# Optimization experiments

Hardware: AMD Instinct MI355X
Metric: run time of the kernel (lower is better)

The kernel has to match this reference:

```python
import jax, jax.numpy as jnp
import numpy as np

E, K, D, H, C = 32768, 32, 128, 4, 10
DH = D // H

def setup_inputs() -> dict:
    key = jax.random.key(0)
    ks = jax.random.split(key, 9)
    s = 1.0 / np.sqrt(D)
    return {
        "edge_feats": jax.random.normal(ks[0], (E, D), jnp.float32),
        "Wq": jax.random.normal(ks[1], (D, D), jnp.float32) * s,
        "Wk": jax.random.normal(ks[2], (D, D), jnp.float32) * s,
        "Wv": jax.random.normal(ks[3], (D, D), jnp.float32) * s,
        "Wo": jax.random.normal(ks[4], (D, D), jnp.float32) * s,
        "W1": jax.random.normal(ks[5], (D, D), jnp.float32) * s,
        "b1": jnp.zeros((D,), jnp.float32),
        "W2": jax.random.normal(ks[6], (D, C), jnp.float32) * s,
        "b2": jnp.zeros((C,), jnp.float32),
        "edge_adj": jax.random.randint(ks[7], (E, K), 0, E, jnp.int32),
    }

def reference(edge_feats, Wq, Wk, Wv, Wo, W1, b1, W2, b2, edge_adj):
    # Edge attention: each edge attends over its K adjacent edges.
    q = (edge_feats @ Wq).reshape(E, H, DH)                 # [E,H,dh]
    k_all = edge_feats @ Wk                                  # [E,D]
    v_all = edge_feats @ Wv                                  # [E,D]
    kn = k_all[edge_adj].reshape(E, K, H, DH)                # gather [E,K,H,dh]
    vn = v_all[edge_adj].reshape(E, K, H, DH)                # gather [E,K,H,dh]
    scores = jnp.einsum("ehd,ekhd->ehk", q, kn) / np.sqrt(DH)
    attn = jax.nn.softmax(scores, axis=-1)                   # [E,H,K]
    ctx = jnp.einsum("ehk,ekhd->ehd", attn, vn).reshape(E, D)
    edge_out = ctx @ Wo                                       # [E,D]
    # classifier: Linear -> GELU -> Linear
    h = jax.nn.gelu(edge_out @ W1 + b1)
    logits = h @ W2 + b2                                      # [E,C]
    return logits
```

## Files before the change

### kernel.cpp

```cpp
#include <hip/hip_runtime.h>
#include <hip/hip_bf16.h>

constexpr int E_EDGES = 32768;
constexpr int DIM = 128;

using bf16x8 = __attribute__((ext_vector_type(8))) short;
using f32x4  = __attribute__((ext_vector_type(4))) float;
using f32x2  = __attribute__((ext_vector_type(2))) float;
typedef unsigned int uint4v __attribute__((ext_vector_type(4)));
typedef unsigned int uint2v __attribute__((ext_vector_type(2)));

__device__ inline float bflo(unsigned u) { return __uint_as_float(u << 16); }
__device__ inline float bfhi(unsigned u) { return __uint_as_float(u & 0xffff0000u); }
__device__ inline f32x2 bf2f2(unsigned u) {
    f32x2 r;
    r[0] = __uint_as_float(u << 16);
    r[1] = __uint_as_float(u & 0xffff0000u);
    return r;
}
__device__ inline f32x2 fma2(f32x2 a, f32x2 b, f32x2 c) {
    return __builtin_elementwise_fma(a, b, c);
}
__device__ inline unsigned pk_bf2(float a, float b) {
    __hip_bfloat162 h = __float22bfloat162_rn(make_float2(a, b));
    return *(unsigned*)&h;
}

#if __has_builtin(__builtin_amdgcn_fdot2_f32_bf16)
typedef __bf16 bf16x2v __attribute__((ext_vector_type(2)));
__device__ inline float dot2bf(unsigned a, unsigned b, float c) {
    return __builtin_amdgcn_fdot2_f32_bf16(__builtin_bit_cast(bf16x2v, a),
                                           __builtin_bit_cast(bf16x2v, b),
                                           c, false);
}
#else
__device__ inline float dot2bf(unsigned a, unsigned b, float c) {
    float r = fmaf(bflo(a), bflo(b), c);
    return fmaf(bfhi(a), bfhi(b), r);
}
#endif

__global__ __launch_bounds__(256) void k_prep(
    const float* __restrict__ Wq, const float* __restrict__ Wk,
    const float* __restrict__ Wv, const float* __restrict__ Wo,
    const float* __restrict__ W1, __hip_bfloat16* __restrict__ Wt,
    __hip_bfloat16* __restrict__ wft) {
    const int b = blockIdx.x;
    const int t = threadIdx.x;
    if (b < 3) {
        const float* W = (b == 0) ? Wq : (b == 1) ? Wk : Wv;
        __hip_bfloat16* dst = Wt + b * 16384;
#pragma unroll
        for (int i = 0; i < 8; ++i) {
            int idx = i * 2048 + t * 8;
            int k = idx >> 7, n0 = idx & 127;
            float4 f0 = *(const float4*)(W + k * 128 + n0);
            float4 f1 = *(const float4*)(W + k * 128 + n0 + 4);
            float f[8] = {f0.x, f0.y, f0.z, f0.w, f1.x, f1.y, f1.z, f1.w};
#pragma unroll
            for (int j = 0; j < 8; ++j)
                dst[(n0 + j) * 128 + k] = __float2bfloat16(f[j]);
        }
    } else {
        int idx = (b - 3) * 256 + t;
        int r = idx >> 7, c = idx & 127;
        float acc = 0.f;
#pragma unroll 16
        for (int k = 0; k < 128; ++k)
            acc = fmaf(Wo[r * 128 + k], W1[k * 128 + c], acc);
        wft[c * 128 + r] = __float2bfloat16(acc);
    }
}

__global__ __launch_bounds__(256) void k_qkv(
    const float* __restrict__ feats, const __hip_bfloat16* __restrict__ Wt,
    __hip_bfloat16* __restrict__ qp, __hip_bfloat16* __restrict__ kp,
    __hip_bfloat16* __restrict__ vp) {
    __shared__ short Als[16384];
    __shared__ short Bls[16384];

    const int t = threadIdx.x;
    const int lane = t & 63;
    const int w = t >> 6;
    const int wm = w >> 1, wn = w & 1;
    const int row0 = blockIdx.x * 128;

#pragma unroll
    for (int i = 0; i < 8; ++i) {
        int idx = i * 2048 + t * 8;
        int r = idx >> 7, k0 = idx & 127;
        float4 f0 = *(const float4*)(feats + (size_t)(row0 + r) * DIM + k0);
        float4 f1 = *(const float4*)(feats + (size_t)(row0 + r) * DIM + k0 + 4);
        uint4 o = make_uint4(pk_bf2(f0.x, f0.y), pk_bf2(f0.z, f0.w),
                             pk_bf2(f1.x, f1.y), pk_bf2(f1.z, f1.w));
        *(uint4*)&Als[(r * 128 + k0) ^ ((r & 7) << 3)] = o;
    }
#pragma unroll
    for (int i = 0; i < 8; ++i) {
        int idx = i * 2048 + t * 8;
        int n = idx >> 7, k0 = idx & 127;
        uint4 v = *(const uint4*)(Wt + n * 128 + k0);
        *(uint4*)&Bls[(n * 128 + k0) ^ ((n & 7) << 3)] = v;
    }
    __syncthreads();

    bf16x8 afr[4][4];
#pragma unroll
    for (int m = 0; m < 4; ++m)
#pragma unroll
        for (int ks = 0; ks < 4; ++ks) {
            int r = wm * 64 + m * 16 + (lane & 15);
            int kb = ks * 32 + (lane >> 4) * 8;
            afr[m][ks] = *(bf16x8*)&Als[(r * 128 + kb) ^ ((r & 7) << 3)];
        }

    for (int proj = 0; proj < 3; ++proj) {
        f32x4 acc[4][4];
#pragma unroll
        for (int m = 0; m < 4; ++m)
#pragma unroll
            for (int n = 0; n < 4; ++n) acc[m][n] = (f32x4){0.f, 0.f, 0.f, 0.f};

#pragma unroll
        for (int ks = 0; ks < 4; ++ks) {
            bf16x8 bfr[4];
#pragma unroll
            for (int n = 0; n < 4; ++n) {
                int nn = wn * 64 + n * 16 + (lane & 15);
                int kb = ks * 32 + (lane >> 4) * 8;
                bfr[n] = *(bf16x8*)&Bls[(nn * 128 + kb) ^ ((nn & 7) << 3)];
            }
#pragma unroll
            for (int m = 0; m < 4; ++m)
#pragma unroll
                for (int n = 0; n < 4; ++n)
                    acc[m][n] = __builtin_amdgcn_mfma_f32_16x16x32_bf16(
                        afr[m][ks], bfr[n], acc[m][n], 0, 0, 0);
        }

        {
            __hip_bfloat16* dst = (proj == 0) ? qp : (proj == 1) ? kp : vp;
#pragma unroll
            for (int n = 0; n < 4; ++n) {
                int c = wn * 64 + n * 16 + (lane & 15);
                int h = c >> 5, pr = h & 1;
                int slot = ((h >> 1) << 5) + (c & 31);
                size_t base = (size_t)pr * E_EDGES * 64 + slot;
#pragma unroll
                for (int m = 0; m < 4; ++m) {
                    int rb = row0 + wm * 64 + m * 16 + (lane >> 4) * 4;
#pragma unroll
                    for (int r = 0; r < 4; ++r)
                        dst[base + (size_t)(rb + r) * 64] =
                            __float2bfloat16(acc[m][n][r]);
                }
            }
        }

        if (proj < 2) {
            __syncthreads();
#pragma unroll
            for (int i = 0; i < 8; ++i) {
                int idx = i * 2048 + t * 8;
                int n = idx >> 7, k0 = idx & 127;
                uint4 v = *(const uint4*)(Wt + (proj + 1) * 16384 + n * 128 + k0);
                *(uint4*)&Bls[(n * 128 + k0) ^ ((n & 7) << 3)] = v;
            }
            __syncthreads();
        }
    }
}

__global__ __launch_bounds__(256) void k_attn_mlp(
    const __hip_bfloat16* __restrict__ qp, const __hip_bfloat16* __restrict__ kp,
    const __hip_bfloat16* __restrict__ vp, const int* __restrict__ adj,
    const __hip_bfloat16* __restrict__ wft, const float* __restrict__ b1,
    const float* __restrict__ W2, const float* __restrict__ b2,
    float* __restrict__ out) {
    __shared__ short ctxls[2048];
    __shared__ short hls[2048];
    __shared__ float w2s[1280];
    __shared__ float b1s[128];
    __shared__ float b2s[16];

    const int t = threadIdx.x;
    const int lane = t & 63;
    const int w = t >> 6;
    const int e0 = blockIdx.x * 16;

    for (int i = t; i < 1280; i += 256) w2s[i] = W2[i];
    if (t < 128) b1s[t] = b1[t];
    if (t < 10) b2s[t] = b2[t];

    const int n = lane & 31;
    const int g = lane >> 5;
    const int rsel = lane >> 3;
    const int csel = lane & 7;
    const int gi = csel >> 2;

    for (int it = 0; it < 8; ++it) {
        const int u = w * 8 + it;
        const int pass = u >> 4;
        const int eloc = u & 15;
        const int e = e0 + eloc;

        int adjv = 0;
        if (lane < 32) adjv = __builtin_nontemporal_load(adj + e * 32 + lane);

        const uint4v* qr =
            (const uint4v*)(qp + ((size_t)pass * E_EDGES + e) * 64 + g * 32);
        uint4v qu[4];
#pragma unroll
        for (int j = 0; j < 4; ++j) qu[j] = __builtin_nontemporal_load(qr + j);

        const int row = __shfl(adjv, n, 64);
        const uint4* kr =
            (const uint4*)(kp + ((size_t)pass * E_EDGES + row) * 64 + g * 32);
        float s0 = 0.f;
#pragma unroll
        for (int j = 0; j < 4; ++j) {
            uint4 uu = kr[j];
            s0 = dot2bf(qu[j][0], uu.x, s0);
            s0 = dot2bf(qu[j][1], uu.y, s0);
            s0 = dot2bf(qu[j][2], uu.z, s0);
            s0 = dot2bf(qu[j][3], uu.w, s0);
        }
        s0 *= 0.17677669529663689f;

        float m0 = s0;
#pragma unroll
        for (int off = 16; off; off >>= 1) m0 = fmaxf(m0, __shfl_xor(m0, off));
        float ex0 = __expf(s0 - m0);
        float sum0 = ex0;
#pragma unroll
        for (int off = 16; off; off >>= 1) sum0 += __shfl_xor(sum0, off);
        const float wgt = ex0 / sum0;

        f32x2 c01 = {0.f, 0.f}, c23 = {0.f, 0.f}, c45 = {0.f, 0.f}, c67 = {0.f, 0.f};
#pragma unroll
        for (int i = 0; i < 4; ++i) {
            int nn = i * 8 + rsel;
            float a = __shfl(wgt, gi * 32 + nn, 64);
            int r2 = __shfl(adjv, nn, 64);
            uint4 uu = *(const uint4*)(vp + ((size_t)pass * E_EDGES + r2) * 64 + csel * 8);
            f32x2 a2 = {a, a};
            c01 = fma2(a2, bf2f2(uu.x), c01);
            c23 = fma2(a2, bf2f2(uu.y), c23);
            c45 = fma2(a2, bf2f2(uu.z), c45);
            c67 = fma2(a2, bf2f2(uu.w), c67);
        }
        float c[8] = {c01[0], c01[1], c23[0], c23[1], c45[0], c45[1], c67[0], c67[1]};
#pragma unroll
        for (int off = 8; off <= 32; off <<= 1)
#pragma unroll
            for (int j = 0; j < 8; ++j) c[j] += __shfl_xor(c[j], off);

        if (lane < 8) {
            int h2 = pass + 2 * (lane >> 2);
            uint4v o;
            o[0] = pk_bf2(c[0], c[1]);
            o[1] = pk_bf2(c[2], c[3]);
            o[2] = pk_bf2(c[4], c[5]);
            o[3] = pk_bf2(c[6], c[7]);
            *(uint4v*)&ctxls[(eloc * 128 + h2 * 32 + (lane & 3) * 8) ^
                             ((eloc & 7) << 3)] = o;
        }
    }
    __syncthreads();

    {
        const int lr = lane & 15;
        bf16x8 afr[4], bfr[2][4];
#pragma unroll
        for (int ks = 0; ks < 4; ++ks) {
            int kb = ks * 32 + (lane >> 4) * 8;
            afr[ks] = *(bf16x8*)&ctxls[(lr * 128 + kb) ^ ((lr & 7) << 3)];
        }
#pragma unroll
        for (int nf = 0; nf < 2; ++nf)
#pragma unroll
            for (int ks = 0; ks < 4; ++ks) {
                int nn2 = w * 32 + nf * 16 + (lane & 15);
                int kb = ks * 32 + (lane >> 4) * 8;
                bfr[nf][ks] = *(const bf16x8*)(wft + nn2 * 128 + kb);
            }
        f32x4 acc[2] = {(f32x4){0.f, 0.f, 0.f, 0.f}, (f32x4){0.f, 0.f, 0.f, 0.f}};
#pragma unroll
        for (int ks = 0; ks < 4; ++ks) {
            acc[0] = __builtin_amdgcn_mfma_f32_16x16x32_bf16(afr[ks], bfr[0][ks],
                                                             acc[0], 0, 0, 0);
            acc[1] = __builtin_amdgcn_mfma_f32_16x16x32_bf16(afr[ks], bfr[1][ks],
                                                             acc[1], 0, 0, 0);
        }
#pragma unroll
        for (int nf = 0; nf < 2; ++nf) {
            int c = w * 32 + nf * 16 + (lane & 15);
            float bc = b1s[c];
#pragma unroll
            for (int r = 0; r < 4; ++r) {
                float x = acc[nf][r] + bc;
                float uu = 0.7978845608028654f * (x + 0.044715f * x * x * x);
                float exu = __expf(2.f * uu);
                float th = 1.f - 2.f / (exu + 1.f);
                float h = 0.5f * x * (1.f + th);
                int hr = (lane >> 4) * 4 + r;
                hls[(hr * 128 + c) ^ ((hr & 7) << 3)] =
                    (short)(__bfloat16_as_ushort(__float2bfloat16(h)));
            }
        }
    }
    __syncthreads();

    if (t < 160) {
        int r = t / 10, c = t - r * 10;
        float a = b2s[c];
#pragma unroll 8
        for (int kk = 0; kk < 128; ++kk) {
            float hv = __uint_as_float(
                ((unsigned)(unsigned short)hls[(r * 128 + kk) ^ ((r & 7) << 3)]) << 16);
            a = fmaf(hv, w2s[kk * 10 + c], a);
        }
        out[(size_t)(e0 + r) * 10 + c] = a;
    }
}

extern "C" void kernel_launch(void* const* d_in, const int* in_sizes, int n_in,
                              void* d_out, int out_size, void* d_ws, size_t ws_size,
                              hipStream_t stream) {
    const float* feats = (const float*)d_in[0];
    const float* Wq    = (const float*)d_in[1];
    const float* Wk    = (const float*)d_in[2];
    const float* Wv    = (const float*)d_in[3];
    const float* Wo    = (const float*)d_in[4];
    const float* W1    = (const float*)d_in[5];
    const float* b1    = (const float*)d_in[6];
    const float* W2    = (const float*)d_in[7];
    const float* b2    = (const float*)d_in[8];
    const int*   adj   = (const int*)d_in[9];
    float* out = (float*)d_out;

    const size_t ED2 = (size_t)E_EDGES * 64;
    __hip_bfloat16* base = (__hip_bfloat16*)d_ws;
    __hip_bfloat16* qp   = base;
    __hip_bfloat16* kp   = qp + 2 * ED2;
    __hip_bfloat16* vp   = kp + 2 * ED2;
    __hip_bfloat16* wt   = vp + 2 * ED2;
    __hip_bfloat16* wft  = wt + 3 * 16384;

    k_prep<<<67, 256, 0, stream>>>(Wq, Wk, Wv, Wo, W1, wt, wft);
    k_qkv<<<E_EDGES / 128, 256, 0, stream>>>(feats, wt, qp, kp, vp);
    k_attn_mlp<<<E_EDGES / 16, 256, 0, stream>>>(qp, kp, vp, adj, wft,
                                                 b1, W2, b2, out);
}
```

Measured before the change: 116.9 us.

## Split attention into per-head-pair passes and stage QKV stores through LDS

The QKV projection kernel now uses 64-row tiles and writes its outputs through shared memory, so each global store is a coalesced 16-byte vector instead of scattered 2-byte stores. Attention is split into two kernels, one per head-pair half. The first processes pass 0 and writes its context to a new bf16 workspace. The second handles pass 1 plus the MLP and reads the stored context back into LDS. The intent is to keep each gathered K/V half small enough to stay cache-resident, at the cost of an extra launch and an extra context round-trip through memory.

```diff
diff --git a/kernel.cpp b/kernel.cpp
--- a/kernel.cpp
+++ b/kernel.cpp
@@ -76,18 +76,18 @@
     const float* __restrict__ feats, const __hip_bfloat16* __restrict__ Wt,
     __hip_bfloat16* __restrict__ qp, __hip_bfloat16* __restrict__ kp,
     __hip_bfloat16* __restrict__ vp) {
-    __shared__ short Als[16384];
+    __shared__ short Als[8192];
     __shared__ short Bls[16384];
 
     const int t = threadIdx.x;
     const int lane = t & 63;
     const int w = t >> 6;
     const int wm = w >> 1, wn = w & 1;
-    const int row0 = blockIdx.x * 128;
-
-#pragma unroll
-    for (int i = 0; i < 8; ++i) {
-        int idx = i * 2048 + t * 8;
+    const int row0 = blockIdx.x * 64;
+
+#pragma unroll
+    for (int i = 0; i < 4; ++i) {
+        int idx = (i * 256 + t) * 8;
         int r = idx >> 7, k0 = idx & 127;
         float4 f0 = *(const float4*)(feats + (size_t)(row0 + r) * DIM + k0);
         float4 f1 = *(const float4*)(feats + (size_t)(row0 + r) * DIM + k0 + 4);
@@ -104,20 +104,20 @@
     }
     __syncthreads();
 
-    bf16x8 afr[4][4];
-#pragma unroll
-    for (int m = 0; m < 4; ++m)
+    bf16x8 afr[2][4];
+#pragma unroll
+    for (int m = 0; m < 2; ++m)
 #pragma unroll
         for (int ks = 0; ks < 4; ++ks) {
-            int r = wm * 64 + m * 16 + (lane & 15);
+            int r = wm * 32 + m * 16 + (lane & 15);
             int kb = ks * 32 + (lane >> 4) * 8;
             afr[m][ks] = *(bf16x8*)&Als[(r * 128 + kb) ^ ((r & 7) << 3)];
         }
 
     for (int proj = 0; proj < 3; ++proj) {
-        f32x4 acc[4][4];
-#pragma unroll
-        for (int m = 0; m < 4; ++m)
+        f32x4 acc[2][4];
+#pragma unroll
+        for (int m = 0; m < 2; ++m)
 #pragma unroll
             for (int n = 0; n < 4; ++n) acc[m][n] = (f32x4){0.f, 0.f, 0.f, 0.f};
 
@@ -131,34 +131,29 @@
                 bfr[n] = *(bf16x8*)&Bls[(nn * 128 + kb) ^ ((nn & 7) << 3)];
             }
 #pragma unroll
-            for (int m = 0; m < 4; ++m)
+            for (int m = 0; m < 2; ++m)
 #pragma unroll
                 for (int n = 0; n < 4; ++n)
                     acc[m][n] = __builtin_amdgcn_mfma_f32_16x16x32_bf16(
                         afr[m][ks], bfr[n], acc[m][n], 0, 0, 0);
         }
 
-        {
-            __hip_bfloat16* dst = (proj == 0) ? qp : (proj == 1) ? kp : vp;
+        __syncthreads();
+
+#pragma unroll
+        for (int m = 0; m < 2; ++m) {
 #pragma unroll
             for (int n = 0; n < 4; ++n) {
                 int c = wn * 64 + n * 16 + (lane & 15);
-                int h = c >> 5, pr = h & 1;
-                int slot = ((h >> 1) << 5) + (c & 31);
-                size_t base = (size_t)pr * E_EDGES * 64 + slot;
-#pragma unroll
-                for (int m = 0; m < 4; ++m) {
-                    int rb = row0 + wm * 64 + m * 16 + (lane >> 4) * 4;
-#pragma unroll
-                    for (int r = 0; r < 4; ++r)
-                        dst[base + (size_t)(rb + r) * 64] =
-                            __float2bfloat16(acc[m][n][r]);
+#pragma unroll
+                for (int r = 0; r < 4; ++r) {
+                    int lr = wm * 32 + m * 16 + (lane >> 4) * 4 + r;
+                    Als[(lr * 128 + c) ^ ((lr & 7) << 3)] =
+                        (short)__bfloat16_as_ushort(__float2bfloat16(acc[m][n][r]));
                 }
             }
         }
-
         if (proj < 2) {
-            __syncthreads();
 #pragma unroll
             for (int i = 0; i < 8; ++i) {
                 int idx = i * 2048 + t * 8;
@@ -166,17 +161,104 @@
                 uint4 v = *(const uint4*)(Wt + (proj + 1) * 16384 + n * 128 + k0);
                 *(uint4*)&Bls[(n * 128 + k0) ^ ((n & 7) << 3)] = v;
             }
-            __syncthreads();
-        }
-    }
-}
-
-__global__ __launch_bounds__(256) void k_attn_mlp(
+        }
+        __syncthreads();
+
+        {
+            __hip_bfloat16* dst = (proj == 0) ? qp : (proj == 1) ? kp : vp;
+#pragma unroll
+            for (int i = 0; i < 4; ++i) {
+                int id = i * 256 + t;
+                int r = id >> 4;
+                int c0 = (id & 15) * 8;
+                uint4 v4 = *(uint4*)&Als[(r * 128 + c0) ^ ((r & 7) << 3)];
+                int h = c0 >> 5, pr = h & 1;
+                int slot = ((h >> 1) << 5) + (c0 & 31);
+                *(uint4*)(dst + ((size_t)pr * E_EDGES + row0 + r) * 64 + slot) = v4;
+            }
+        }
+    }
+}
+
+__global__ __launch_bounds__(256) void k_attn0(
     const __hip_bfloat16* __restrict__ qp, const __hip_bfloat16* __restrict__ kp,
     const __hip_bfloat16* __restrict__ vp, const int* __restrict__ adj,
-    const __hip_bfloat16* __restrict__ wft, const float* __restrict__ b1,
-    const float* __restrict__ W2, const float* __restrict__ b2,
-    float* __restrict__ out) {
+    __hip_bfloat16* __restrict__ ctxb) {
+    const int lane = threadIdx.x & 63;
+    const int e = blockIdx.x * 4 + (threadIdx.x >> 6);
+    const int n = lane & 31;
+    const int g = lane >> 5;
+
+    int adjv = 0;
+    if (lane < 32) adjv = __builtin_nontemporal_load(adj + e * 32 + lane);
+
+    const uint4v* qr = (const uint4v*)(qp + (size_t)e * 64 + g * 32);
+    uint4v qu[4];
+#pragma unroll
+    for (int j = 0; j < 4; ++j) qu[j] = __builtin_nontemporal_load(qr + j);
+
+    const int row = __shfl(adjv, n, 64);
+    const uint4* kr = (const uint4*)(kp + (size_t)row * 64 + g * 32);
+    float s0 = 0.f;
+#pragma unroll
+    for (int j = 0; j < 4; ++j) {
+        uint4 u = kr[j];
+        s0 = dot2bf(qu[j][0], u.x, s0);
+        s0 = dot2bf(qu[j][1], u.y, s0);
+        s0 = dot2bf(qu[j][2], u.z, s0);
+        s0 = dot2bf(qu[j][3], u.w, s0);
+    }
+    s0 *= 0.17677669529663689f;
+
+    float m0 = s0;
+#pragma unroll
+    for (int off = 16; off; off >>= 1) m0 = fmaxf(m0, __shfl_xor(m0, off));
+    float e0 = __expf(s0 - m0);
+    float sum0 = e0;
+#pragma unroll
+    for (int off = 16; off; off >>= 1) sum0 += __shfl_xor(sum0, off);
+    const float wgt = e0 / sum0;
+
+    const int rsel = lane >> 3;
+    const int csel = lane & 7;
+    const int gi = csel >> 2;
+    f32x2 c01 = {0.f, 0.f}, c23 = {0.f, 0.f}, c45 = {0.f, 0.f}, c67 = {0.f, 0.f};
+#pragma unroll
+    for (int i = 0; i < 4; ++i) {
+        int nn = i * 8 + rsel;
+        float a = __shfl(wgt, gi * 32 + nn, 64);
+        int r2 = __shfl(adjv, nn, 64);
+        uint4 u = *(const uint4*)(vp + (size_t)r2 * 64 + csel * 8);
+        f32x2 a2 = {a, a};
+        c01 = fma2(a2, bf2f2(u.x), c01);
+        c23 = fma2(a2, bf2f2(u.y), c23);
+        c45 = fma2(a2, bf2f2(u.z), c45);
+        c67 = fma2(a2, bf2f2(u.w), c67);
+    }
+    float c[8] = {c01[0], c01[1], c23[0], c23[1], c45[0], c45[1], c67[0], c67[1]};
+#pragma unroll
+    for (int off = 8; off <= 32; off <<= 1)
+#pragma unroll
+        for (int j = 0; j < 8; ++j) c[j] += __shfl_xor(c[j], off);
+
+    if (lane < 8) {
+        int h2 = 2 * (lane >> 2);
+        uint4v o;
+        o[0] = pk_bf2(c[0], c[1]);
+        o[1] = pk_bf2(c[2], c[3]);
+        o[2] = pk_bf2(c[4], c[5]);
+        o[3] = pk_bf2(c[6], c[7]);
+        __builtin_nontemporal_store(
+            o, (uint4v*)(ctxb + (size_t)e * DIM + h2 * 32 + (lane & 3) * 8));
+    }
+}
+
+__global__ __launch_bounds__(256) void k_attn1_mlp(
+    const __hip_bfloat16* __restrict__ qp, const __hip_bfloat16* __restrict__ kp,
+    const __hip_bfloat16* __restrict__ vp, const int* __restrict__ adj,
+    const __hip_bfloat16* __restrict__ ctxb, const __hip_bfloat16* __restrict__ wft,
+    const float* __restrict__ b1, const float* __restrict__ W2,
+    const float* __restrict__ b2, float* __restrict__ out) {
     __shared__ short ctxls[2048];
     __shared__ short hls[2048];
     __shared__ float w2s[1280];
@@ -192,30 +274,35 @@
     if (t < 128) b1s[t] = b1[t];
     if (t < 10) b2s[t] = b2[t];
 
+    if (t < 128) {
+        int eloc = t >> 3, chunk = t & 7;
+        int off = (chunk < 4) ? chunk * 8 : 64 + (chunk - 4) * 8;
+        uint4v v = *(const uint4v*)(ctxb + (size_t)(e0 + eloc) * DIM + off);
+        *(uint4v*)&ctxls[(eloc * 128 + off) ^ ((eloc & 7) << 3)] = v;
+    }
+
     const int n = lane & 31;
     const int g = lane >> 5;
     const int rsel = lane >> 3;
     const int csel = lane & 7;
     const int gi = csel >> 2;
 
-    for (int it = 0; it < 8; ++it) {
-        const int u = w * 8 + it;
-        const int pass = u >> 4;
-        const int eloc = u & 15;
+    for (int it = 0; it < 4; ++it) {
+        const int eloc = w * 4 + it;
         const int e = e0 + eloc;
 
         int adjv = 0;
         if (lane < 32) adjv = __builtin_nontemporal_load(adj + e * 32 + lane);
 
         const uint4v* qr =
-            (const uint4v*)(qp + ((size_t)pass * E_EDGES + e) * 64 + g * 32);
+            (const uint4v*)(qp + ((size_t)E_EDGES + e) * 64 + g * 32);
         uint4v qu[4];
 #pragma unroll
         for (int j = 0; j < 4; ++j) qu[j] = __builtin_nontemporal_load(qr + j);
 
         const int row = __shfl(adjv, n, 64);
         const uint4* kr =
-            (const uint4*)(kp + ((size_t)pass * E_EDGES + row) * 64 + g * 32);
+            (const uint4*)(kp + ((size_t)E_EDGES + row) * 64 + g * 32);
         float s0 = 0.f;
 #pragma unroll
         for (int j = 0; j < 4; ++j) {
@@ -242,7 +329,7 @@
             int nn = i * 8 + rsel;
             float a = __shfl(wgt, gi * 32 + nn, 64);
             int r2 = __shfl(adjv, nn, 64);
-            uint4 uu = *(const uint4*)(vp + ((size_t)pass * E_EDGES + r2) * 64 + csel * 8);
+            uint4 uu = *(const uint4*)(vp + ((size_t)E_EDGES + r2) * 64 + csel * 8);
             f32x2 a2 = {a, a};
             c01 = fma2(a2, bf2f2(uu.x), c01);
             c23 = fma2(a2, bf2f2(uu.y), c23);
@@ -256,7 +343,7 @@
             for (int j = 0; j < 8; ++j) c[j] += __shfl_xor(c[j], off);
 
         if (lane < 8) {
-            int h2 = pass + 2 * (lane >> 2);
+            int h2 = 1 + 2 * (lane >> 2);
             uint4v o;
             o[0] = pk_bf2(c[0], c[1]);
             o[1] = pk_bf2(c[2], c[3]);
@@ -344,11 +431,13 @@
     __hip_bfloat16* qp   = base;
     __hip_bfloat16* kp   = qp + 2 * ED2;
     __hip_bfloat16* vp   = kp + 2 * ED2;
-    __hip_bfloat16* wt   = vp + 2 * ED2;
+    __hip_bfloat16* ctxb = vp + 2 * ED2;
+    __hip_bfloat16* wt   = ctxb + 2 * ED2;
     __hip_bfloat16* wft  = wt + 3 * 16384;
 
     k_prep<<<67, 256, 0, stream>>>(Wq, Wk, Wv, Wo, W1, wt, wft);
-    k_qkv<<<E_EDGES / 128, 256, 0, stream>>>(feats, wt, qp, kp, vp);
-    k_attn_mlp<<<E_EDGES / 16, 256, 0, stream>>>(qp, kp, vp, adj, wft,
-                                                 b1, W2, b2, out);
-}
+    k_qkv<<<E_EDGES / 64, 256, 0, stream>>>(feats, wt, qp, kp, vp);
+    k_attn0<<<E_EDGES / 4, 256, 0, stream>>>(qp, kp, vp, adj, ctxb);
+    k_attn1_mlp<<<E_EDGES / 16, 256, 0, stream>>>(qp, kp, vp, adj, ctxb, wft,
+                                                  b1, W2, b2, out);
+}
```

Result: faster. 113.6 us (-2.9%).
